# Kernel optimization log

Measured on AMD Instinct MI355X. Metric: run time of the kernel, lower is better.

Reference implementation:

```python
import jax, jax.numpy as jnp
import numpy as np

L, H, D, FF = 6, 16, 768, 3072
B, N = 4, 1023
HD = D // H  # 48
EPS = 1e-5


def _layernorm(x, w, b):
    m = jnp.mean(x, axis=-1, keepdims=True)
    v = jnp.mean((x - m) ** 2, axis=-1, keepdims=True)
    return (x - m) / jnp.sqrt(v + EPS) * w + b


def setup_inputs() -> dict:
    key = jax.random.key(0)
    ks = jax.random.split(key, 10)
    ratio = 2.0 ** (-8.0 / H)
    slopes = np.array([ratio ** (i + 1) for i in range(H)], dtype=np.float32)
    return {
        "cls_tokens": jax.random.normal(ks[0], (B, N, D), jnp.float32),
        "cls_token": jax.random.normal(ks[1], (1, 1, D), jnp.float32) * 0.02,
        "log_slopes": jnp.log(jnp.asarray(slopes)),
        "Wqkv": jax.random.normal(ks[2], (L, 3 * D, D), jnp.float32) * 0.02,
        "Wo": jax.random.normal(ks[3], (L, D, D), jnp.float32) * 0.02,
        "Wg": jax.random.normal(ks[4], (L, FF, D), jnp.float32) * 0.02,
        "Wu": jax.random.normal(ks[5], (L, FF, D), jnp.float32) * 0.02,
        "Wd": jax.random.normal(ks[6], (L, D, FF), jnp.float32) * 0.02,
        "ln1_w": jnp.ones((L, D), jnp.float32),
        "ln1_b": jnp.zeros((L, D), jnp.float32),
        "ln2_w": jnp.ones((L, D), jnp.float32),
        "ln2_b": jnp.zeros((L, D), jnp.float32),
        "fin_w": jnp.ones((D,), jnp.float32),
        "fin_b": jnp.zeros((D,), jnp.float32),
    }


def reference(cls_tokens, cls_token, log_slopes, Wqkv, Wo, Wg, Wu, Wd,
              ln1_w, ln1_b, ln2_w, ln2_b, fin_w, fin_b):
    b, n, dmodel = cls_tokens.shape
    S = n + 1
    # learnable ALiBi: -exp(log_slope) * |i - j|, shape (H, S, S)
    pos = jnp.arange(S)
    dist = jnp.abs(pos[None, :] - pos[:, None]).astype(cls_tokens.dtype)
    bias = -(jnp.exp(log_slopes)[:, None, None] * dist[None, :, :])

    x = jnp.concatenate([jnp.broadcast_to(cls_token, (b, 1, dmodel)), cls_tokens], axis=1)
    scale = 1.0 / jnp.sqrt(jnp.asarray(HD, x.dtype))

    for l in range(L):
        h = _layernorm(x, ln1_w[l], ln1_b[l])
        qkv = jnp.einsum('bsd,ed->bse', h, Wqkv[l]).reshape(b, S, 3, H, HD)
        qkv = qkv.transpose(2, 0, 3, 1, 4)  # (3, B, H, S, hd)
        q, k, v = qkv[0], qkv[1], qkv[2]
        scores = jnp.einsum('bhqd,bhkd->bhqk', q, k) * scale + bias[None]
        attn = jax.nn.softmax(scores, axis=-1)
        o = jnp.einsum('bhqk,bhkd->bhqd', attn, v)
        o = o.transpose(0, 2, 1, 3).reshape(b, S, dmodel)
        x = x + jnp.einsum('bsd,ed->bse', o, Wo[l])
        h = _layernorm(x, ln2_w[l], ln2_b[l])
        gate = jax.nn.silu(jnp.einsum('bsd,fd->bsf', h, Wg[l]))
        up = jnp.einsum('bsd,fd->bsf', h, Wu[l])
        x = x + jnp.einsum('bsf,df->bsd', gate * up, Wd[l])

    return _layernorm(x[:, 0, :], fin_w, fin_b)
```

## Files before the change

### kernel.cpp

```cpp
#include <hip/hip_runtime.h>
#include <hip/hip_bf16.h>

#define LNUM 6
#define HNUM 16
#define DMODEL 768
#define FFDIM 3072
#define BATCH 4
#define NTOK 1023
#define SEQ 1024
#define HD 48
#define EPS 1e-5f

typedef __hip_bfloat16 bf16;

__device__ __forceinline__ unsigned short f2bf_raw(float f) {
  bf16 h = __float2bfloat16(f);
  union { bf16 h; unsigned short s; } u; u.h = h; return u.s;
}

template <int CTRL>
__device__ __forceinline__ float dppf(float x) {
  return __int_as_float(__builtin_amdgcn_update_dpp(
      0, __float_as_int(x), CTRL, 0xf, 0xf, true));
}
__device__ __forceinline__ float row_max16(float x) {
  x = fmaxf(x, dppf<0xB1>(x));
  x = fmaxf(x, dppf<0x4E>(x));
  x = fmaxf(x, dppf<0x124>(x));
  x = fmaxf(x, dppf<0x128>(x));
  return x;
}
__device__ __forceinline__ float row_sum16(float x) {
  x += dppf<0xB1>(x);
  x += dppf<0x4E>(x);
  x += dppf<0x124>(x);
  x += dppf<0x128>(x);
  return x;
}

__global__ __launch_bounds__(256) void concat_kernel(
    const float* __restrict__ cls_tokens, const float* __restrict__ cls_token,
    float* __restrict__ x) {
  size_t i = (size_t)blockIdx.x * blockDim.x + threadIdx.x;
  const size_t total = (size_t)BATCH * SEQ * DMODEL;
  if (i >= total) return;
  int d = (int)(i % DMODEL);
  size_t bs = i / DMODEL;
  int s = (int)(bs % SEQ);
  int b = (int)(bs / SEQ);
  float v;
  if (s == 0) v = cls_token[d];
  else v = cls_tokens[((size_t)b * NTOK + (s - 1)) * DMODEL + d];
  x[i] = v;
}

#define W_QKV4  442368
#define W_O4    147456
#define W_FF4   589824
__global__ __launch_bounds__(256) void convert_w_kernel(
    const float* __restrict__ wqkv, const float* __restrict__ wo,
    const float* __restrict__ wg, const float* __restrict__ wu,
    const float* __restrict__ wd, bf16* __restrict__ dst) {
  size_t i4 = (size_t)blockIdx.x * 256 + threadIdx.x;
  size_t off4 = i4;
  const float* src;
  if (off4 < W_QKV4) src = wqkv;
  else { off4 -= W_QKV4;
    if (off4 < W_O4) src = wo;
    else { off4 -= W_O4;
      if (off4 < W_FF4) src = wg;
      else { off4 -= W_FF4;
        if (off4 < W_FF4) src = wu;
        else { off4 -= W_FF4; src = wd; } } } }
  float4 v = ((const float4*)src)[off4];
  ushort4 o;
  o.x = f2bf_raw(v.x); o.y = f2bf_raw(v.y);
  o.z = f2bf_raw(v.z); o.w = f2bf_raw(v.w);
  ((ushort4*)dst)[i4] = o;
}

__device__ __forceinline__ void st_ln(float* p, float v) { *p = v; }
__device__ __forceinline__ void st_ln(bf16* p, float v) { *p = __float2bfloat16(v); }

template <typename OUT>
__global__ __launch_bounds__(256) void ln_kernel(
    const float* __restrict__ in, OUT* __restrict__ out,
    const float* __restrict__ w, const float* __restrict__ bias,
    size_t in_stride, size_t out_stride) {
  const int row = blockIdx.x;
  const int tid = threadIdx.x;
  const float* x = in + (size_t)row * in_stride;
  OUT* y = out + (size_t)row * out_stride;

  float v0 = x[tid], v1 = x[tid + 256], v2 = x[tid + 512];
  float s = v0 + v1 + v2;
  float sq = v0 * v0 + v1 * v1 + v2 * v2;

  __shared__ float s_sum[256];
  __shared__ float s_sq[256];
  s_sum[tid] = s;
  s_sq[tid] = sq;
  __syncthreads();
  for (int off = 128; off > 0; off >>= 1) {
    if (tid < off) {
      s_sum[tid] += s_sum[tid + off];
      s_sq[tid] += s_sq[tid + off];
    }
    __syncthreads();
  }
  const float inv_d = 1.0f / (float)DMODEL;
  float mean = s_sum[0] * inv_d;
  float var = s_sq[0] * inv_d - mean * mean;
  float rstd = rsqrtf(var + EPS);

  st_ln(y + tid,       (v0 - mean) * rstd * w[tid]       + bias[tid]);
  st_ln(y + tid + 256, (v1 - mean) * rstd * w[tid + 256] + bias[tid + 256]);
  st_ln(y + tid + 512, (v2 - mean) * rstd * w[tid + 512] + bias[tid + 512]);
}

#define BM 128
#define BN 128
#define BK 32

typedef __attribute__((ext_vector_type(8))) short bfrag;
typedef __attribute__((ext_vector_type(4))) float f32x4;

__device__ __forceinline__ void async_copy16(const void* g, void* l) {
  __builtin_amdgcn_global_load_lds(
      (const __attribute__((address_space(1))) void*)g,
      (__attribute__((address_space(3))) void*)l, 16, 0, 0);
}

template <int CMODE>
__global__ __launch_bounds__(256) void gemm_bf16(
    const bf16* __restrict__ A, const bf16* __restrict__ B,
    void* __restrict__ Cv, int M, int N, int K) {
  __shared__ bf16 As[2][BM][BK];
  __shared__ bf16 Bs[2][BN][BK];

  const int tid = threadIdx.x;
  const int wave = tid >> 6;
  const int lane = tid & 63;
  const int m0 = blockIdx.y * BM;
  const int n0 = blockIdx.x * BN;
  const int wm = (wave & 1) * 64;
  const int wn = (wave >> 1) * 64;

  f32x4 acc[4][4];
#pragma unroll
  for (int i = 0; i < 4; i++)
#pragma unroll
    for (int j = 0; j < 4; j++) acc[i][j] = (f32x4)(0.f);

  const int lrow = lane >> 2;
  const int lcol = (lane & 3) * 8;
  const bf16* Ag[2]; const bf16* Bg[2];
  void *AsB[2][2], *BsB[2][2];
#pragma unroll
  for (int j = 0; j < 2; j++) {
    int c = j * 4 + wave;
    Ag[j] = A + (size_t)(m0 + c * 16 + lrow) * K + lcol;
    Bg[j] = B + (size_t)(n0 + c * 16 + lrow) * K + lcol;
#pragma unroll
    for (int bf = 0; bf < 2; bf++) {
      AsB[bf][j] = (void*)&As[bf][c * 16][0];
      BsB[bf][j] = (void*)&Bs[bf][c * 16][0];
    }
  }

#pragma unroll
  for (int j = 0; j < 2; j++) {
    async_copy16(Ag[j], AsB[0][j]);
    async_copy16(Bg[j], BsB[0][j]);
  }

  const int fr = lane & 15;
  const int fk = (lane >> 4) * 8;
  const int nk = K / BK;

  for (int ki = 0; ki < nk; ki++) {
    const int cur = ki & 1;
    __syncthreads();
    if (ki + 1 < nk) {
      const int k0 = (ki + 1) * BK;
#pragma unroll
      for (int j = 0; j < 2; j++) {
        async_copy16(Ag[j] + k0, AsB[cur ^ 1][j]);
        async_copy16(Bg[j] + k0, BsB[cur ^ 1][j]);
      }
    }
    bfrag a[4], b[4];
#pragma unroll
    for (int i = 0; i < 4; i++) {
      a[i] = *(const bfrag*)&As[cur][wm + i * 16 + fr][fk];
      b[i] = *(const bfrag*)&Bs[cur][wn + i * 16 + fr][fk];
    }
#pragma unroll
    for (int i = 0; i < 4; i++)
#pragma unroll
      for (int j = 0; j < 4; j++)
        acc[i][j] = __builtin_amdgcn_mfma_f32_16x16x32_bf16(a[i], b[j], acc[i][j], 0, 0, 0);
  }

  const int ccol = lane & 15;
  const int crow = (lane >> 4) * 4;
#pragma unroll
  for (int i = 0; i < 4; i++) {
#pragma unroll
    for (int j = 0; j < 4; j++) {
#pragma unroll
      for (int r = 0; r < 4; r++) {
        const size_t gm = m0 + wm + i * 16 + crow + r;
        const size_t gn = n0 + wn + j * 16 + ccol;
        if (CMODE == 2) {
          ((bf16*)Cv)[gm * N + gn] = __float2bfloat16(acc[i][j][r]);
        } else if (CMODE == 1) {
          float* cp = (float*)Cv + gm * N + gn;
          *cp += acc[i][j][r];
        } else {
          ((float*)Cv)[gm * N + gn] = acc[i][j][r];
        }
      }
    }
  }
}

template <int CMODE>
__global__ __launch_bounds__(256) void gemm_bf16_n64(
    const bf16* __restrict__ A, const bf16* __restrict__ B,
    void* __restrict__ Cv, int M, int N, int K) {
  __shared__ bf16 As[2][64][BK];
  __shared__ bf16 Bs[2][64][BK];

  const int tid = threadIdx.x;
  const int wave = tid >> 6;
  const int lane = tid & 63;
  const int m0 = blockIdx.y * 64;
  const int n0 = blockIdx.x * 64;
  const int wm = (wave & 1) * 32;
  const int wn = (wave >> 1) * 32;

  f32x4 acc[2][2];
#pragma unroll
  for (int i = 0; i < 2; i++)
#pragma unroll
    for (int j = 0; j < 2; j++) acc[i][j] = (f32x4)(0.f);

  const int srow = tid >> 2;
  const int scol = (tid & 3) * 8;
  const bf16* Ag = A + (size_t)(m0 + srow) * K + scol;
  const bf16* Bg = B + (size_t)(n0 + srow) * K + scol;
  void *AsB[2], *BsB[2];
#pragma unroll
  for (int bf = 0; bf < 2; bf++) {
    AsB[bf] = (void*)&As[bf][srow][scol];
    BsB[bf] = (void*)&Bs[bf][srow][scol];
  }

  async_copy16(Ag, AsB[0]);
  async_copy16(Bg, BsB[0]);

  const int fr = lane & 15;
  const int fk = (lane >> 4) * 8;
  const int nk = K / BK;

  for (int ki = 0; ki < nk; ki++) {
    const int cur = ki & 1;
    __syncthreads();
    if (ki + 1 < nk) {
      const int k0 = (ki + 1) * BK;
      async_copy16(Ag + k0, AsB[cur ^ 1]);
      async_copy16(Bg + k0, BsB[cur ^ 1]);
    }
    bfrag a[2], b[2];
#pragma unroll
    for (int i = 0; i < 2; i++)
      a[i] = *(const bfrag*)&As[cur][wm + i * 16 + fr][fk];
#pragma unroll
    for (int j = 0; j < 2; j++)
      b[j] = *(const bfrag*)&Bs[cur][wn + j * 16 + fr][fk];
#pragma unroll
    for (int i = 0; i < 2; i++)
#pragma unroll
      for (int j = 0; j < 2; j++)
        acc[i][j] = __builtin_amdgcn_mfma_f32_16x16x32_bf16(a[i], b[j], acc[i][j], 0, 0, 0);
  }

  const int ccol = lane & 15;
  const int crow = (lane >> 4) * 4;
#pragma unroll
  for (int i = 0; i < 2; i++) {
#pragma unroll
    for (int j = 0; j < 2; j++) {
#pragma unroll
      for (int r = 0; r < 4; r++) {
        const size_t gm = m0 + wm + i * 16 + crow + r;
        const size_t gn = n0 + wn + j * 16 + ccol;
        if (CMODE == 2) {
          ((bf16*)Cv)[gm * N + gn] = __float2bfloat16(acc[i][j][r]);
        } else if (CMODE == 1) {
          float* cp = (float*)Cv + gm * N + gn;
          *cp += acc[i][j][r];
        } else {
          ((float*)Cv)[gm * N + gn] = acc[i][j][r];
        }
      }
    }
  }
}

__global__ __launch_bounds__(256) void gemm_gateup(
    const bf16* __restrict__ A, const bf16* __restrict__ Wg,
    const bf16* __restrict__ Wu, bf16* __restrict__ gu, int M, int N, int K) {
  __shared__ bf16 As[2][BM][BK];
  __shared__ bf16 Gs[2][BN][BK];
  __shared__ bf16 Us[2][BN][BK];

  const int tid = threadIdx.x;
  const int wave = tid >> 6;
  const int lane = tid & 63;
  const int m0 = blockIdx.y * BM;
  const int n0 = blockIdx.x * BN;
  const int wm = (wave & 1) * 64;
  const int wn = (wave >> 1) * 64;

  f32x4 accG[4][4], accU[4][4];
#pragma unroll
  for (int i = 0; i < 4; i++)
#pragma unroll
    for (int j = 0; j < 4; j++) { accG[i][j] = (f32x4)(0.f); accU[i][j] = (f32x4)(0.f); }

  const int lrow = lane >> 2;
  const int lcol = (lane & 3) * 8;
  const bf16 *Ag[2], *Gg[2], *Ug[2];
  void *AsB[2][2], *GsB[2][2], *UsB[2][2];
#pragma unroll
  for (int j = 0; j < 2; j++) {
    int c = j * 4 + wave;
    Ag[j] = A + (size_t)(m0 + c * 16 + lrow) * K + lcol;
    Gg[j] = Wg + (size_t)(n0 + c * 16 + lrow) * K + lcol;
    Ug[j] = Wu + (size_t)(n0 + c * 16 + lrow) * K + lcol;
#pragma unroll
    for (int bf = 0; bf < 2; bf++) {
      AsB[bf][j] = (void*)&As[bf][c * 16][0];
      GsB[bf][j] = (void*)&Gs[bf][c * 16][0];
      UsB[bf][j] = (void*)&Us[bf][c * 16][0];
    }
  }

#pragma unroll
  for (int j = 0; j < 2; j++) {
    async_copy16(Ag[j], AsB[0][j]);
    async_copy16(Gg[j], GsB[0][j]);
    async_copy16(Ug[j], UsB[0][j]);
  }

  const int fr = lane & 15;
  const int fk = (lane >> 4) * 8;
  const int nk = K / BK;

  for (int ki = 0; ki < nk; ki++) {
    const int cur = ki & 1;
    __syncthreads();
    if (ki + 1 < nk) {
      const int k0 = (ki + 1) * BK;
#pragma unroll
      for (int j = 0; j < 2; j++) {
        async_copy16(Ag[j] + k0, AsB[cur ^ 1][j]);
        async_copy16(Gg[j] + k0, GsB[cur ^ 1][j]);
        async_copy16(Ug[j] + k0, UsB[cur ^ 1][j]);
      }
    }
    bfrag a[4], g[4], u[4];
#pragma unroll
    for (int i = 0; i < 4; i++) {
      a[i] = *(const bfrag*)&As[cur][wm + i * 16 + fr][fk];
      g[i] = *(const bfrag*)&Gs[cur][wn + i * 16 + fr][fk];
      u[i] = *(const bfrag*)&Us[cur][wn + i * 16 + fr][fk];
    }
#pragma unroll
    for (int i = 0; i < 4; i++)
#pragma unroll
      for (int j = 0; j < 4; j++) {
        accG[i][j] = __builtin_amdgcn_mfma_f32_16x16x32_bf16(a[i], g[j], accG[i][j], 0, 0, 0);
        accU[i][j] = __builtin_amdgcn_mfma_f32_16x16x32_bf16(a[i], u[j], accU[i][j], 0, 0, 0);
      }
  }

  const int ccol = lane & 15;
  const int crow = (lane >> 4) * 4;
#pragma unroll
  for (int i = 0; i < 4; i++) {
#pragma unroll
    for (int j = 0; j < 4; j++) {
#pragma unroll
      for (int r = 0; r < 4; r++) {
        const size_t gm = m0 + wm + i * 16 + crow + r;
        const size_t gn = n0 + wn + j * 16 + ccol;
        const float gv = accG[i][j][r];
        const float uv = accU[i][j][r];
        const float res = gv / (1.0f + __expf(-gv)) * uv;
        gu[gm * N + gn] = __float2bfloat16(res);
      }
    }
  }
}

__global__ __launch_bounds__(256) void transpose_v(
    const bf16* __restrict__ qkv, bf16* __restrict__ vt) {
  __shared__ bf16 T[HD][64];
  const int tid = threadIdx.x;
  const int kb = blockIdx.x * 64;
  const int h = blockIdx.y;
  const int b = blockIdx.z;
  const size_t rstride = 3 * DMODEL;
  const bf16* vsrc = qkv + ((size_t)(b * SEQ + kb)) * rstride + 2 * DMODEL + h * HD;

  if (tid < 192) {
    int p = tid & 31, c = tid >> 5;
    const bf16* v0 = vsrc + (size_t)(2 * p) * rstride + c * 8;
    uint4 r0 = *(const uint4*)v0;
    uint4 r1 = *(const uint4*)(v0 + rstride);
    const unsigned int* w0 = (const unsigned int*)&r0;
    const unsigned int* w1 = (const unsigned int*)&r1;
#pragma unroll
    for (int i = 0; i < 8; i++) {
      unsigned int lo = (i & 1) ? (w0[i >> 1] >> 16) : (w0[i >> 1] & 0xffffu);
      unsigned int hi = (i & 1) ? (w1[i >> 1] >> 16) : (w1[i >> 1] & 0xffffu);
      *(unsigned int*)&T[c * 8 + i][2 * p] = lo | (hi << 16);
    }
  }
  __syncthreads();
  for (int it = tid; it < HD * 8; it += 256) {
    int d = it >> 3, c = it & 7;
    *(uint4*)(vt + ((size_t)((b * HNUM + h) * HD + d)) * SEQ + kb + c * 8) =
        *(const uint4*)&T[d][c * 8];
  }
}

#define AQT 64
#define AKT 64
#define ASTR 72

__global__ __launch_bounds__(256, 4) void attn_mfma(
    const bf16* __restrict__ qkv, const bf16* __restrict__ vt,
    const float* __restrict__ log_slopes, bf16* __restrict__ obuf) {
  __shared__ bf16 Qs[AQT][ASTR];
  __shared__ bf16 Ks[AKT][ASTR];
  __shared__ bf16 Vs[HD][ASTR];
  __shared__ bf16 Pt[AQT][ASTR];

  const int tid = threadIdx.x;
  const int wq = tid >> 6;
  const int lane = tid & 63;
  const int l15 = lane & 15;
  const int lh = lane >> 4;

  const int id = blockIdx.x;
  const int w = (id & 7) * 128 + (id >> 3);
  const int qb = (w & 15) * AQT;
  const int h = (w >> 4) & 15;
  const int b = w >> 8;

  const float c1 = 0.14433756729740643f * 1.4426950408889634f;
  const float slope2 = __expf(log_slopes[h]) * 1.4426950408889634f;
  const size_t rstride = 3 * DMODEL;
  const bf16* qbase = qkv + ((size_t)(b * SEQ + qb)) * rstride + h * HD;
  const bf16* kbase0 = qkv + ((size_t)b * SEQ) * rstride + DMODEL + h * HD;
  const bf16* vbase0 = vt + ((size_t)((b * HNUM + h) * HD)) * SEQ;

  bf16* ldst[3];
  size_t goff[3];
  bool isK[3];
#pragma unroll
  for (int j = 0; j < 3; j++) {
    int id2 = tid + j * 256;
    if (id2 < 384) {
      int r = id2 / 6, c = id2 - r * 6;
      ldst[j] = &Ks[r][c * 8];
      goff[j] = (size_t)r * rstride + c * 8;
      isK[j] = true;
    } else {
      id2 -= 384;
      int d = id2 >> 3, c = id2 & 7;
      ldst[j] = &Vs[d][c * 8];
      goff[j] = (size_t)d * SEQ + c * 8;
      isK[j] = false;
    }
  }

  for (int it = tid; it < AQT * 2; it += 256) {
    int r = it >> 1, c = it & 1;
    *(uint4*)&Qs[r][48 + c * 8] = make_uint4(0, 0, 0, 0);
    *(uint4*)&Ks[r][48 + c * 8] = make_uint4(0, 0, 0, 0);
  }
  for (int it = tid; it < AQT * 6; it += 256) {
    int r = it / 6, c = it - (it / 6) * 6;
    *(uint4*)&Qs[r][c * 8] = *(const uint4*)(qbase + (size_t)r * rstride + c * 8);
  }

  uint4 pre[3];
#pragma unroll
  for (int j = 0; j < 3; j++)
    pre[j] = *(const uint4*)((isK[j] ? kbase0 : vbase0) + goff[j]);

  float m_[4], l_[4];
  f32x4 accO[3];
#pragma unroll
  for (int r = 0; r < 4; r++) { m_[r] = -1e30f; l_[r] = 0.f; }
#pragma unroll
  for (int t = 0; t < 3; t++) accO[t] = (f32x4)(0.f);

  for (int kb = 0; kb < SEQ; kb += AKT) {
    __syncthreads();
#pragma unroll
    for (int j = 0; j < 3; j++) *(uint4*)ldst[j] = pre[j];
    __syncthreads();
    if (kb + AKT < SEQ) {
      const bf16* kb1 = kbase0 + (size_t)(kb + AKT) * rstride;
      const bf16* vb1 = vbase0 + (kb + AKT);
#pragma unroll
      for (int j = 0; j < 3; j++)
        pre[j] = *(const uint4*)((isK[j] ? kb1 : vb1) + goff[j]);
    }

    f32x4 accS[4];
#pragma unroll
    for (int j = 0; j < 4; j++) accS[j] = (f32x4)(0.f);
    __builtin_amdgcn_s_setprio(1);
#pragma unroll
    for (int ks = 0; ks < 2; ks++) {
      bfrag a = *(const bfrag*)&Qs[wq * 16 + l15][ks * 32 + lh * 8];
#pragma unroll
      for (int j = 0; j < 4; j++) {
        bfrag bk = *(const bfrag*)&Ks[j * 16 + l15][ks * 32 + lh * 8];
        accS[j] = __builtin_amdgcn_mfma_f32_16x16x32_bf16(a, bk, accS[j], 0, 0, 0);
      }
    }
    __builtin_amdgcn_s_setprio(0);

    float ps[4][4];
#pragma unroll
    for (int r = 0; r < 4; r++) {
      const float fq = (float)(qb + wq * 16 + lh * 4 + r);
      float s[4];
#pragma unroll
      for (int j = 0; j < 4; j++) {
        const float fk = (float)(kb + j * 16 + l15);
        const float t = slope2 * fabsf(fq - fk);
        s[j] = fmaf(accS[j][r], c1, -t);
      }
      float mx = row_max16(fmaxf(fmaxf(s[0], s[1]), fmaxf(s[2], s[3])));
      const float mnew = fmaxf(m_[r], mx);
      const float corr = exp2f(m_[r] - mnew);
      float rs = 0.f;
#pragma unroll
      for (int j = 0; j < 4; j++) {
        ps[j][r] = exp2f(s[j] - mnew);
        rs += ps[j][r];
      }
      rs = row_sum16(rs);
      l_[r] = l_[r] * corr + rs;
      m_[r] = mnew;
#pragma unroll
      for (int t = 0; t < 3; t++) accO[t][r] *= corr;
    }

#pragma unroll
    for (int j = 0; j < 4; j++)
#pragma unroll
      for (int r = 0; r < 4; r++)
        Pt[wq * 16 + lh * 4 + r][j * 16 + l15] = __float2bfloat16(ps[j][r]);

#pragma unroll
    for (int ks = 0; ks < 2; ks++) {
      bfrag pa = *(const bfrag*)&Pt[wq * 16 + l15][ks * 32 + lh * 8];
      __builtin_amdgcn_s_setprio(1);
#pragma unroll
      for (int t = 0; t < 3; t++) {
        bfrag vb = *(const bfrag*)&Vs[t * 16 + l15][ks * 32 + lh * 8];
        accO[t] = __builtin_amdgcn_mfma_f32_16x16x32_bf16(pa, vb, accO[t], 0, 0, 0);
      }
      __builtin_amdgcn_s_setprio(0);
    }
  }

#pragma unroll
  for (int r = 0; r < 4; r++) {
    const float inv = 1.0f / l_[r];
    bf16* op = obuf + ((size_t)(b * SEQ + qb + wq * 16 + lh * 4 + r)) * DMODEL + h * HD;
#pragma unroll
    for (int t = 0; t < 3; t++)
      op[t * 16 + l15] = __float2bfloat16(accO[t][r] * inv);
  }
}

extern "C" void kernel_launch(void* const* d_in, const int* in_sizes, int n_in,
                              void* d_out, int out_size, void* d_ws, size_t ws_size,
                              hipStream_t stream) {
  const float* cls_tokens = (const float*)d_in[0];
  const float* cls_token  = (const float*)d_in[1];
  const float* log_slopes = (const float*)d_in[2];
  const float* Wqkv = (const float*)d_in[3];
  const float* Wo   = (const float*)d_in[4];
  const float* Wg   = (const float*)d_in[5];
  const float* Wu   = (const float*)d_in[6];
  const float* Wd   = (const float*)d_in[7];
  const float* ln1_w = (const float*)d_in[8];
  const float* ln1_b = (const float*)d_in[9];
  const float* ln2_w = (const float*)d_in[10];
  const float* ln2_b = (const float*)d_in[11];
  const float* fin_w = (const float*)d_in[12];
  const float* fin_b = (const float*)d_in[13];
  float* out = (float*)d_out;

  const size_t ROWS = (size_t)BATCH * SEQ;
  char* wsb = (char*)d_ws;
  float* x    = (float*)(wsb);
  bf16* qkvb  = (bf16*)(wsb + 12582912);
  bf16* hb    = (bf16*)(wsb + 31457280);
  bf16* ob    = (bf16*)(wsb + 37748736);
  bf16* gub   = (bf16*)(wsb + 44040192);
  bf16* wbf   = (bf16*)(wsb + 94371840);
  bf16* vtb   = (bf16*)(wsb + 113246208);

  bf16* wqkv_b = wbf;
  bf16* wo_b   = wbf + 1769472;
  bf16* wg_b   = wbf + 2359296;
  bf16* wu_b   = wbf + 4718592;
  bf16* wd_b   = wbf + 7077888;

  {
    const size_t total = ROWS * DMODEL;
    concat_kernel<<<(int)((total + 255) / 256), 256, 0, stream>>>(cls_tokens, cls_token, x);
  }

  for (int l = 0; l < LNUM; l++) {
    convert_w_kernel<<<9216, 256, 0, stream>>>(
        Wqkv + (size_t)l * 3 * DMODEL * DMODEL, Wo + (size_t)l * DMODEL * DMODEL,
        Wg + (size_t)l * FFDIM * DMODEL, Wu + (size_t)l * FFDIM * DMODEL,
        Wd + (size_t)l * DMODEL * FFDIM, wbf);

    ln_kernel<bf16><<<(int)ROWS, 256, 0, stream>>>(
        x, hb, ln1_w + l * DMODEL, ln1_b + l * DMODEL, DMODEL, DMODEL);
    gemm_bf16<2><<<dim3(3 * DMODEL / BN, ROWS / BM), 256, 0, stream>>>(
        hb, wqkv_b, qkvb, (int)ROWS, 3 * DMODEL, DMODEL);
    transpose_v<<<dim3(SEQ / 64, HNUM, BATCH), 256, 0, stream>>>(qkvb, vtb);
    attn_mfma<<<dim3(SEQ / AQT * HNUM * BATCH), 256, 0, stream>>>(
        qkvb, vtb, log_slopes, ob);
    gemm_bf16_n64<1><<<dim3(DMODEL / 64, ROWS / 64), 256, 0, stream>>>(
        ob, wo_b, x, (int)ROWS, DMODEL, DMODEL);
    ln_kernel<bf16><<<(int)ROWS, 256, 0, stream>>>(
        x, hb, ln2_w + l * DMODEL, ln2_b + l * DMODEL, DMODEL, DMODEL);
    gemm_gateup<<<dim3(FFDIM / BN, ROWS / BM), 256, 0, stream>>>(
        hb, wg_b, wu_b, gub, (int)ROWS, FFDIM, DMODEL);
    gemm_bf16_n64<1><<<dim3(DMODEL / 64, ROWS / 64), 256, 0, stream>>>(
        gub, wd_b, x, (int)ROWS, DMODEL, FFDIM);
  }

  ln_kernel<float><<<BATCH, 256, 0, stream>>>(x, out, fin_w, fin_b,
                                              (size_t)SEQ * DMODEL, DMODEL);
}
```

Baseline: 1.754 ms.

## Add XCD block swizzle, split-K down projection, and larger attention key tiles

```diff
diff --git a/kernel.cpp b/kernel.cpp
--- a/kernel.cpp
+++ b/kernel.cpp
@@ -36,6 +36,15 @@
   x += dppf<0x124>(x);
   x += dppf<0x128>(x);
   return x;
+}
+
+__device__ __forceinline__ void xcd_swz(int& bx, int& by) {
+  const int gx = gridDim.x;
+  const int lin = blockIdx.y * gx + blockIdx.x;
+  const int cpx = (gx * gridDim.y) >> 3;
+  const int w = (lin & 7) * cpx + (lin >> 3);
+  bx = w % gx;
+  by = w / gx;
 }
 
 __global__ __launch_bounds__(256) void concat_kernel(
@@ -141,8 +150,10 @@
   const int tid = threadIdx.x;
   const int wave = tid >> 6;
   const int lane = tid & 63;
-  const int m0 = blockIdx.y * BM;
-  const int n0 = blockIdx.x * BN;
+  int bx, by;
+  xcd_swz(bx, by);
+  const int m0 = by * BM;
+  const int n0 = bx * BN;
   const int wm = (wave & 1) * 64;
   const int wn = (wave >> 1) * 64;
 
@@ -225,7 +236,7 @@
   }
 }
 
-template <int CMODE>
+template <int CMODE, int SPLITK>
 __global__ __launch_bounds__(256) void gemm_bf16_n64(
     const bf16* __restrict__ A, const bf16* __restrict__ B,
     void* __restrict__ Cv, int M, int N, int K) {
@@ -235,10 +246,13 @@
   const int tid = threadIdx.x;
   const int wave = tid >> 6;
   const int lane = tid & 63;
-  const int m0 = blockIdx.y * 64;
-  const int n0 = blockIdx.x * 64;
+  int bx, by;
+  xcd_swz(bx, by);
+  const int m0 = by * 64;
+  const int n0 = bx * 64;
   const int wm = (wave & 1) * 32;
   const int wn = (wave >> 1) * 32;
+  const int koff = (SPLITK > 1) ? (int)blockIdx.z * (K / SPLITK) : 0;
 
   f32x4 acc[2][2];
 #pragma unroll
@@ -248,8 +262,8 @@
 
   const int srow = tid >> 2;
   const int scol = (tid & 3) * 8;
-  const bf16* Ag = A + (size_t)(m0 + srow) * K + scol;
-  const bf16* Bg = B + (size_t)(n0 + srow) * K + scol;
+  const bf16* Ag = A + (size_t)(m0 + srow) * K + koff + scol;
+  const bf16* Bg = B + (size_t)(n0 + srow) * K + koff + scol;
   void *AsB[2], *BsB[2];
 #pragma unroll
   for (int bf = 0; bf < 2; bf++) {
@@ -262,7 +276,7 @@
 
   const int fr = lane & 15;
   const int fk = (lane >> 4) * 8;
-  const int nk = K / BK;
+  const int nk = (K / SPLITK) / BK;
 
   for (int ki = 0; ki < nk; ki++) {
     const int cur = ki & 1;
@@ -300,7 +314,8 @@
           ((bf16*)Cv)[gm * N + gn] = __float2bfloat16(acc[i][j][r]);
         } else if (CMODE == 1) {
           float* cp = (float*)Cv + gm * N + gn;
-          *cp += acc[i][j][r];
+          if (SPLITK > 1) atomicAdd(cp, acc[i][j][r]);
+          else *cp += acc[i][j][r];
         } else {
           ((float*)Cv)[gm * N + gn] = acc[i][j][r];
         }
@@ -319,8 +334,10 @@
   const int tid = threadIdx.x;
   const int wave = tid >> 6;
   const int lane = tid & 63;
-  const int m0 = blockIdx.y * BM;
-  const int n0 = blockIdx.x * BN;
+  int bx, by;
+  xcd_swz(bx, by);
+  const int m0 = by * BM;
+  const int n0 = bx * BN;
   const int wm = (wave & 1) * 64;
   const int wn = (wave >> 1) * 64;
 
@@ -439,16 +456,16 @@
 }
 
 #define AQT 64
-#define AKT 64
+#define AKT 128
 #define ASTR 72
+#define VSTR 136
 
 __global__ __launch_bounds__(256, 4) void attn_mfma(
     const bf16* __restrict__ qkv, const bf16* __restrict__ vt,
     const float* __restrict__ log_slopes, bf16* __restrict__ obuf) {
-  __shared__ bf16 Qs[AQT][ASTR];
+  __shared__ bf16 QPs[AQT][ASTR];
   __shared__ bf16 Ks[AKT][ASTR];
-  __shared__ bf16 Vs[HD][ASTR];
-  __shared__ bf16 Pt[AQT][ASTR];
+  __shared__ bf16 Vs[HD][VSTR];
 
   const int tid = threadIdx.x;
   const int wq = tid >> 6;
@@ -469,40 +486,43 @@
   const bf16* kbase0 = qkv + ((size_t)b * SEQ) * rstride + DMODEL + h * HD;
   const bf16* vbase0 = vt + ((size_t)((b * HNUM + h) * HD)) * SEQ;
 
-  bf16* ldst[3];
-  size_t goff[3];
-  bool isK[3];
-#pragma unroll
-  for (int j = 0; j < 3; j++) {
-    int id2 = tid + j * 256;
-    if (id2 < 384) {
+  bf16* ldst[6];
+  int goff[6];
+#pragma unroll
+  for (int j = 0; j < 6; j++) {
+    if (j < 3) {
+      int id2 = tid + j * 256;
       int r = id2 / 6, c = id2 - r * 6;
       ldst[j] = &Ks[r][c * 8];
-      goff[j] = (size_t)r * rstride + c * 8;
-      isK[j] = true;
+      goff[j] = r * (int)rstride + c * 8;
     } else {
-      id2 -= 384;
-      int d = id2 >> 3, c = id2 & 7;
+      int id3 = tid + (j - 3) * 256;
+      int d = id3 >> 4, c = id3 & 15;
       ldst[j] = &Vs[d][c * 8];
-      goff[j] = (size_t)d * SEQ + c * 8;
-      isK[j] = false;
-    }
-  }
-
-  for (int it = tid; it < AQT * 2; it += 256) {
-    int r = it >> 1, c = it & 1;
-    *(uint4*)&Qs[r][48 + c * 8] = make_uint4(0, 0, 0, 0);
+      goff[j] = d * SEQ + c * 8;
+    }
+  }
+
+  {
+    int r = tid >> 1, c = tid & 1;
     *(uint4*)&Ks[r][48 + c * 8] = make_uint4(0, 0, 0, 0);
+  }
+  if (tid < 128) {
+    int r = tid >> 1, c = tid & 1;
+    *(uint4*)&QPs[r][48 + c * 8] = make_uint4(0, 0, 0, 0);
   }
   for (int it = tid; it < AQT * 6; it += 256) {
     int r = it / 6, c = it - (it / 6) * 6;
-    *(uint4*)&Qs[r][c * 8] = *(const uint4*)(qbase + (size_t)r * rstride + c * 8);
-  }
-
-  uint4 pre[3];
-#pragma unroll
-  for (int j = 0; j < 3; j++)
-    pre[j] = *(const uint4*)((isK[j] ? kbase0 : vbase0) + goff[j]);
+    *(uint4*)&QPs[r][c * 8] = *(const uint4*)(qbase + (size_t)r * rstride + c * 8);
+  }
+  __syncthreads();
+  const bfrag aq0 = *(const bfrag*)&QPs[wq * 16 + l15][lh * 8];
+  const bfrag aq1 = *(const bfrag*)&QPs[wq * 16 + l15][32 + lh * 8];
+
+  uint4 pre[6];
+#pragma unroll
+  for (int j = 0; j < 6; j++)
+    pre[j] = *(const uint4*)((j < 3 ? kbase0 : vbase0) + goff[j]);
 
   float m_[4], l_[4];
   f32x4 accO[3];
@@ -514,48 +534,49 @@
   for (int kb = 0; kb < SEQ; kb += AKT) {
     __syncthreads();
 #pragma unroll
-    for (int j = 0; j < 3; j++) *(uint4*)ldst[j] = pre[j];
+    for (int j = 0; j < 6; j++) *(uint4*)ldst[j] = pre[j];
     __syncthreads();
     if (kb + AKT < SEQ) {
       const bf16* kb1 = kbase0 + (size_t)(kb + AKT) * rstride;
       const bf16* vb1 = vbase0 + (kb + AKT);
 #pragma unroll
-      for (int j = 0; j < 3; j++)
-        pre[j] = *(const uint4*)((isK[j] ? kb1 : vb1) + goff[j]);
-    }
-
-    f32x4 accS[4];
-#pragma unroll
-    for (int j = 0; j < 4; j++) accS[j] = (f32x4)(0.f);
+      for (int j = 0; j < 6; j++)
+        pre[j] = *(const uint4*)((j < 3 ? kb1 : vb1) + goff[j]);
+    }
+
+    f32x4 accS[8];
+#pragma unroll
+    for (int j = 0; j < 8; j++) accS[j] = (f32x4)(0.f);
     __builtin_amdgcn_s_setprio(1);
 #pragma unroll
-    for (int ks = 0; ks < 2; ks++) {
-      bfrag a = *(const bfrag*)&Qs[wq * 16 + l15][ks * 32 + lh * 8];
-#pragma unroll
-      for (int j = 0; j < 4; j++) {
-        bfrag bk = *(const bfrag*)&Ks[j * 16 + l15][ks * 32 + lh * 8];
-        accS[j] = __builtin_amdgcn_mfma_f32_16x16x32_bf16(a, bk, accS[j], 0, 0, 0);
-      }
+    for (int j = 0; j < 8; j++) {
+      bfrag bk = *(const bfrag*)&Ks[j * 16 + l15][lh * 8];
+      accS[j] = __builtin_amdgcn_mfma_f32_16x16x32_bf16(aq0, bk, accS[j], 0, 0, 0);
+    }
+#pragma unroll
+    for (int j = 0; j < 8; j++) {
+      bfrag bk = *(const bfrag*)&Ks[j * 16 + l15][32 + lh * 8];
+      accS[j] = __builtin_amdgcn_mfma_f32_16x16x32_bf16(aq1, bk, accS[j], 0, 0, 0);
     }
     __builtin_amdgcn_s_setprio(0);
 
-    float ps[4][4];
+    float ps[8][4];
 #pragma unroll
     for (int r = 0; r < 4; r++) {
       const float fq = (float)(qb + wq * 16 + lh * 4 + r);
-      float s[4];
-#pragma unroll
-      for (int j = 0; j < 4; j++) {
-        const float fk = (float)(kb + j * 16 + l15);
-        const float t = slope2 * fabsf(fq - fk);
-        s[j] = fmaf(accS[j][r], c1, -t);
-      }
-      float mx = row_max16(fmaxf(fmaxf(s[0], s[1]), fmaxf(s[2], s[3])));
+      const float d0 = fq - (float)(kb + l15);
+      float s[8];
+#pragma unroll
+      for (int j = 0; j < 8; j++)
+        s[j] = fmaf(accS[j][r], c1, -slope2 * fabsf(d0 - 16.0f * (float)j));
+      float mx = fmaxf(fmaxf(fmaxf(s[0], s[1]), fmaxf(s[2], s[3])),
+                       fmaxf(fmaxf(s[4], s[5]), fmaxf(s[6], s[7])));
+      mx = row_max16(mx);
       const float mnew = fmaxf(m_[r], mx);
       const float corr = exp2f(m_[r] - mnew);
       float rs = 0.f;
 #pragma unroll
-      for (int j = 0; j < 4; j++) {
+      for (int j = 0; j < 8; j++) {
         ps[j][r] = exp2f(s[j] - mnew);
         rs += ps[j][r];
       }
@@ -567,21 +588,24 @@
     }
 
 #pragma unroll
-    for (int j = 0; j < 4; j++)
-#pragma unroll
-      for (int r = 0; r < 4; r++)
-        Pt[wq * 16 + lh * 4 + r][j * 16 + l15] = __float2bfloat16(ps[j][r]);
-
-#pragma unroll
-    for (int ks = 0; ks < 2; ks++) {
-      bfrag pa = *(const bfrag*)&Pt[wq * 16 + l15][ks * 32 + lh * 8];
-      __builtin_amdgcn_s_setprio(1);
-#pragma unroll
-      for (int t = 0; t < 3; t++) {
-        bfrag vb = *(const bfrag*)&Vs[t * 16 + l15][ks * 32 + lh * 8];
-        accO[t] = __builtin_amdgcn_mfma_f32_16x16x32_bf16(pa, vb, accO[t], 0, 0, 0);
-      }
-      __builtin_amdgcn_s_setprio(0);
+    for (int half = 0; half < 2; half++) {
+#pragma unroll
+      for (int j2 = 0; j2 < 4; j2++)
+#pragma unroll
+        for (int r = 0; r < 4; r++)
+          QPs[wq * 16 + lh * 4 + r][j2 * 16 + l15] =
+              __float2bfloat16(ps[half * 4 + j2][r]);
+#pragma unroll
+      for (int ks = 0; ks < 2; ks++) {
+        bfrag pa = *(const bfrag*)&QPs[wq * 16 + l15][ks * 32 + lh * 8];
+        __builtin_amdgcn_s_setprio(1);
+#pragma unroll
+        for (int t = 0; t < 3; t++) {
+          bfrag vb = *(const bfrag*)&Vs[t * 16 + l15][half * 64 + ks * 32 + lh * 8];
+          accO[t] = __builtin_amdgcn_mfma_f32_16x16x32_bf16(pa, vb, accO[t], 0, 0, 0);
+        }
+        __builtin_amdgcn_s_setprio(0);
+      }
     }
   }
 
@@ -648,13 +672,13 @@
     transpose_v<<<dim3(SEQ / 64, HNUM, BATCH), 256, 0, stream>>>(qkvb, vtb);
     attn_mfma<<<dim3(SEQ / AQT * HNUM * BATCH), 256, 0, stream>>>(
         qkvb, vtb, log_slopes, ob);
-    gemm_bf16_n64<1><<<dim3(DMODEL / 64, ROWS / 64), 256, 0, stream>>>(
+    gemm_bf16_n64<1, 1><<<dim3(DMODEL / 64, ROWS / 64), 256, 0, stream>>>(
         ob, wo_b, x, (int)ROWS, DMODEL, DMODEL);
     ln_kernel<bf16><<<(int)ROWS, 256, 0, stream>>>(
         x, hb, ln2_w + l * DMODEL, ln2_b + l * DMODEL, DMODEL, DMODEL);
     gemm_gateup<<<dim3(FFDIM / BN, ROWS / BM), 256, 0, stream>>>(
         hb, wg_b, wu_b, gub, (int)ROWS, FFDIM, DMODEL);
-    gemm_bf16_n64<1><<<dim3(DMODEL / 64, ROWS / 64), 256, 0, stream>>>(
+    gemm_bf16_n64<1, 2><<<dim3(DMODEL / 64, ROWS / 64, 2), 256, 0, stream>>>(
         gub, wd_b, x, (int)ROWS, DMODEL, FFDIM);
   }
 
```

Result: slower. 1.790 ms (+2.1%).
